# Optimization experiments

Measured on AMD Instinct MI355X. Metric: run time of the kernel, lower is better.

Reference implementation:

```python
import jax, jax.numpy as jnp
import numpy as np

Q = 127.0
EPS = 1e-8

def act_quant_per_token(x):
    # per-token absmax scale over last dim
    s = jnp.max(jnp.abs(x), axis=-1, keepdims=True) / Q
    s = jnp.maximum(s, EPS)
    xq = jnp.clip(jnp.round(x / s), -Q, Q)
    return xq * s

def ternary_quant(w):
    gamma = jnp.maximum(jnp.mean(jnp.abs(w)), 1e-6)
    wq = jnp.round(jnp.clip(w / gamma, -1.0, 1.0))
    return wq * gamma

def setup_inputs() -> dict:
    key = jax.random.key(0)
    k1, k2 = jax.random.split(key)
    x = jax.random.normal(k1, (4, 2048, 4096), dtype=jnp.float32)
    weight = jax.random.normal(k2, (16384, 4096), dtype=jnp.float32) * 0.02
    return {"x": x, "weight": weight}

def reference(x, weight):
    xq = act_quant_per_token(x)            # [B, S, D]
    wq = ternary_quant(weight)             # [O, D]
    return jnp.einsum('bsd,od->bso', xq, wq)  # [B, S, O]
```

## Files before the change

### kernel.cpp

```cpp
#include <hip/hip_runtime.h>
#include <stdint.h>


#define M_DIM 8192
#define N_DIM 16384
#define K_DIM 4096
#define W_ELEMS (N_DIM * K_DIM)
#define X_ELEMS (M_DIM * K_DIM)

typedef int v4i __attribute__((ext_vector_type(4)));

#define WS_GSUM   0u
#define WS_SCALES 256u
#define WS_XQ     65536u
#define WS_WQ     33685504u

__global__ __launch_bounds__(256) void k_gamma(const float4* __restrict__ w,
                                               double* __restrict__ gsum) {
    int tid = blockIdx.x * 256 + threadIdx.x;
    int stride = gridDim.x * 256;
    float s = 0.f;
    for (int i = tid; i < W_ELEMS / 4; i += stride) {
        float4 v = w[i];
        s += fabsf(v.x) + fabsf(v.y) + fabsf(v.z) + fabsf(v.w);
    }
    #pragma unroll
    for (int off = 32; off; off >>= 1) s += __shfl_down(s, off, 64);
    __shared__ float wsum[4];
    int lane = threadIdx.x & 63, wv = threadIdx.x >> 6;
    if (lane == 0) wsum[wv] = s;
    __syncthreads();
    if (threadIdx.x == 0) {
        double t = (double)wsum[0] + (double)wsum[1] + (double)wsum[2] + (double)wsum[3];
        atomicAdd(gsum, t);
    }
}

__device__ __forceinline__ int pack4i8(float a, float b, float c, float d) {
    int ia = (int)a & 0xFF, ib = (int)b & 0xFF, ic = (int)c & 0xFF, id = (int)d & 0xFF;
    return ia | (ib << 8) | (ic << 16) | (id << 24);
}

__global__ __launch_bounds__(256) void k_wq(const float4* __restrict__ w,
                                            const double* __restrict__ gsum,
                                            int* __restrict__ wq4) {
    float g = fmaxf((float)(*gsum * (1.0 / 67108864.0)), 1e-6f);
    int tid = blockIdx.x * 256 + threadIdx.x;
    int stride = gridDim.x * 256;
    for (int i = tid; i < W_ELEMS / 4; i += stride) {
        float4 v = w[i];
        float qa = rintf(fminf(fmaxf(v.x / g, -1.f), 1.f));
        float qb = rintf(fminf(fmaxf(v.y / g, -1.f), 1.f));
        float qc = rintf(fminf(fmaxf(v.z / g, -1.f), 1.f));
        float qd = rintf(fminf(fmaxf(v.w / g, -1.f), 1.f));
        wq4[i] = pack4i8(qa, qb, qc, qd);
    }
}

__global__ __launch_bounds__(256) void k_xq(const float4* __restrict__ x,
                                            int* __restrict__ xq4,
                                            float* __restrict__ scales) {
    int token = blockIdx.x;
    int t = threadIdx.x;
    const float4* xrow = x + (size_t)token * (K_DIM / 4);
    float4 v[4];
    float m = 0.f;
    #pragma unroll
    for (int i = 0; i < 4; i++) {
        v[i] = xrow[i * 256 + t];
        m = fmaxf(m, fmaxf(fmaxf(fabsf(v[i].x), fabsf(v[i].y)),
                           fmaxf(fabsf(v[i].z), fabsf(v[i].w))));
    }
    #pragma unroll
    for (int off = 32; off; off >>= 1) m = fmaxf(m, __shfl_xor(m, off, 64));
    __shared__ float wm[4];
    int lane = t & 63, wv = t >> 6;
    if (lane == 0) wm[wv] = m;
    __syncthreads();
    m = fmaxf(fmaxf(wm[0], wm[1]), fmaxf(wm[2], wm[3]));
    float s = fmaxf(m / 127.0f, 1e-8f);
    int* orow = xq4 + (size_t)token * (K_DIM / 4);
    #pragma unroll
    for (int i = 0; i < 4; i++) {
        float qa = fminf(fmaxf(rintf(v[i].x / s), -127.f), 127.f);
        float qb = fminf(fmaxf(rintf(v[i].y / s), -127.f), 127.f);
        float qc = fminf(fmaxf(rintf(v[i].z / s), -127.f), 127.f);
        float qd = fminf(fmaxf(rintf(v[i].w / s), -127.f), 127.f);
        orow[i * 256 + t] = pack4i8(qa, qb, qc, qd);
    }
    if (t == 0) scales[token] = s;
}

#define ASYNC_CP16(g, l)                                                              \
    __builtin_amdgcn_global_load_lds((const __attribute__((address_space(1))) void*)(g), \
                                     (__attribute__((address_space(3))) void*)(l), 16, 0, 0)

__global__ __launch_bounds__(256) void k_gemm(const char* __restrict__ A,
                                              const char* __restrict__ B,
                                              const float* __restrict__ scales,
                                              const double* __restrict__ gsum,
                                              float* __restrict__ C) {
    __shared__ char As[128 * 64];
    __shared__ char Bs[128 * 64];
    const int t = threadIdx.x;
    const int m0 = blockIdx.y * 128;
    const int n0 = blockIdx.x * 128;

    const char* aA0 = A + (size_t)(m0 + (t >> 2)) * K_DIM + (t & 3) * 16;
    const char* aA1 = A + (size_t)(m0 + 64 + (t >> 2)) * K_DIM + (t & 3) * 16;
    const char* aB0 = B + (size_t)(n0 + (t >> 2)) * K_DIM + (t & 3) * 16;
    const char* aB1 = B + (size_t)(n0 + 64 + (t >> 2)) * K_DIM + (t & 3) * 16;
    char* lA0 = &As[t * 16];
    char* lA1 = &As[4096 + t * 16];
    char* lB0 = &Bs[t * 16];
    char* lB1 = &Bs[4096 + t * 16];

    v4i acc[4][4];
    #pragma unroll
    for (int i = 0; i < 4; i++)
        #pragma unroll
        for (int j = 0; j < 4; j++) {
            v4i z = {0, 0, 0, 0};
            acc[i][j] = z;
        }

    const int lane = t & 63;
    const int wv = t >> 6;
    const int qm = (wv >> 1) * 64;
    const int qn = (wv & 1) * 64;
    const int r16 = lane & 15;
    const int kq = lane >> 4;

    for (int kk = 0; kk < K_DIM; kk += 64) {
        ASYNC_CP16(aA0 + kk, lA0);
        ASYNC_CP16(aA1 + kk, lA1);
        ASYNC_CP16(aB0 + kk, lB0);
        ASYNC_CP16(aB1 + kk, lB1);
        __syncthreads();
        v4i af[4], bf[4];
        #pragma unroll
        for (int i = 0; i < 4; i++)
            af[i] = *(const v4i*)&As[(qm + i * 16 + r16) * 64 + kq * 16];
        #pragma unroll
        for (int j = 0; j < 4; j++)
            bf[j] = *(const v4i*)&Bs[(qn + j * 16 + r16) * 64 + kq * 16];
        #pragma unroll
        for (int i = 0; i < 4; i++)
            #pragma unroll
            for (int j = 0; j < 4; j++)
                acc[i][j] = __builtin_amdgcn_mfma_i32_16x16x64_i8(af[i], bf[j], acc[i][j], 0, 0, 0);
        __syncthreads();
    }

    float gamma = fmaxf((float)(*gsum * (1.0 / 67108864.0)), 1e-6f);
    #pragma unroll
    for (int i = 0; i < 4; i++) {
        #pragma unroll
        for (int r = 0; r < 4; r++) {
            int grow = m0 + qm + i * 16 + kq * 4 + r;
            float sv = scales[grow] * gamma;
            #pragma unroll
            for (int j = 0; j < 4; j++) {
                int gcol = n0 + qn + j * 16 + r16;
                C[(size_t)grow * N_DIM + gcol] = sv * (float)acc[i][j][r];
            }
        }
    }
}

extern "C" void kernel_launch(void* const* d_in, const int* in_sizes, int n_in,
                              void* d_out, int out_size, void* d_ws, size_t ws_size,
                              hipStream_t stream) {
    const float* x = (const float*)d_in[0];
    const float* w = (const float*)d_in[1];
    float* out = (float*)d_out;
    char* ws = (char*)d_ws;

    double* gsum = (double*)(ws + WS_GSUM);
    float* scales = (float*)(ws + WS_SCALES);
    char* xq = ws + WS_XQ;
    char* wq = ws + WS_WQ;

    hipMemsetAsync(gsum, 0, sizeof(double), stream);
    k_gamma<<<2048, 256, 0, stream>>>((const float4*)w, gsum);
    k_wq<<<4096, 256, 0, stream>>>((const float4*)w, gsum, (int*)wq);
    k_xq<<<M_DIM, 256, 0, stream>>>((const float4*)x, (int*)xq, scales);
    k_gemm<<<dim3(N_DIM / 128, M_DIM / 128), 256, 0, stream>>>(xq, wq, scales, gsum, out);
}
```

Measured before the change: 1.393 ms.

## Rewrite int8 GEMM with 256x256 tiles and 4-stage async LDS pipeline

Replaces the single-buffered 128x128 int8 MFMA GEMM with a 256x256 tile computed by 8 waves, each covering 128x64. Global-to-LDS async copies are issued three k-steps ahead into a 4-deep ring buffer, with explicit vmcnt waits and raw barriers. An XOR swizzle on the LDS layout avoids bank conflicts, and MFMA phases run at raised wave priority. This aims to hide memory latency and increase operand reuse, at the cost of 128 KB of LDS per block, which limits occupancy to one block per CU.

Measured after the change: 1.279 ms. -8.2%, faster.

```diff
diff --git a/kernel.cpp b/kernel.cpp
--- a/kernel.cpp
+++ b/kernel.cpp
@@ -91,81 +91,128 @@
     if (t == 0) scales[token] = s;
 }
 
+
+#define BK 64
+#define NT (K_DIM / BK)
+
 #define ASYNC_CP16(g, l)                                                              \
     __builtin_amdgcn_global_load_lds((const __attribute__((address_space(1))) void*)(g), \
                                      (__attribute__((address_space(3))) void*)(l), 16, 0, 0)
-
-__global__ __launch_bounds__(256) void k_gemm(const char* __restrict__ A,
-                                              const char* __restrict__ B,
-                                              const float* __restrict__ scales,
-                                              const double* __restrict__ gsum,
-                                              float* __restrict__ C) {
-    __shared__ char As[128 * 64];
-    __shared__ char Bs[128 * 64];
+#define WAITV(n) asm volatile("s_waitcnt vmcnt(" #n ")" ::: "memory")
+#define BARRIER() do { asm volatile("" ::: "memory");       \
+                       __builtin_amdgcn_s_barrier();        \
+                       asm volatile("" ::: "memory"); } while (0)
+
+__global__ __launch_bounds__(512, 2) void k_gemm(const char* __restrict__ A,
+                                                 const char* __restrict__ B,
+                                                 const float* __restrict__ scales,
+                                                 const double* __restrict__ gsum,
+                                                 float* __restrict__ C) {
+    __shared__ __align__(16) char As[4][256 * BK];
+    __shared__ __align__(16) char Bs[4][256 * BK];
+
     const int t = threadIdx.x;
-    const int m0 = blockIdx.y * 128;
-    const int n0 = blockIdx.x * 128;
-
-    const char* aA0 = A + (size_t)(m0 + (t >> 2)) * K_DIM + (t & 3) * 16;
-    const char* aA1 = A + (size_t)(m0 + 64 + (t >> 2)) * K_DIM + (t & 3) * 16;
-    const char* aB0 = B + (size_t)(n0 + (t >> 2)) * K_DIM + (t & 3) * 16;
-    const char* aB1 = B + (size_t)(n0 + 64 + (t >> 2)) * K_DIM + (t & 3) * 16;
-    char* lA0 = &As[t * 16];
-    char* lA1 = &As[4096 + t * 16];
-    char* lB0 = &Bs[t * 16];
-    char* lB1 = &Bs[4096 + t * 16];
-
-    v4i acc[4][4];
-    #pragma unroll
-    for (int i = 0; i < 4; i++)
+    const int w = t >> 6;
+    const int l = t & 63;
+    const int m0 = blockIdx.y * 256;
+    const int n0 = blockIdx.x * 256;
+
+    const int srow = l >> 2;
+    const int sslot = (l & 3) ^ ((l >> 3) & 3);
+    const char* gA0 = A + (size_t)(m0 + w * 16 + srow) * K_DIM + sslot * 16;
+    const char* gA1 = gA0 + (size_t)128 * K_DIM;
+    const char* gB0 = B + (size_t)(n0 + w * 16 + srow) * K_DIM + sslot * 16;
+    const char* gB1 = gB0 + (size_t)128 * K_DIM;
+    const int ldsOff = w * 1024 + l * 16;
+
+#define STAGE_A(kt, buf) do {                              \
+        ASYNC_CP16(gA0 + (size_t)(kt) * BK, &As[buf][ldsOff]);        \
+        ASYNC_CP16(gA1 + (size_t)(kt) * BK, &As[buf][8192 + ldsOff]); } while (0)
+#define STAGE_B(kt, buf) do {                              \
+        ASYNC_CP16(gB0 + (size_t)(kt) * BK, &Bs[buf][ldsOff]);        \
+        ASYNC_CP16(gB1 + (size_t)(kt) * BK, &Bs[buf][8192 + ldsOff]); } while (0)
+
+    const int wm = w >> 2;
+    const int wn = w & 3;
+    const int r16 = l & 15;
+    const int kq = l >> 4;
+    const int swz = ((kq ^ ((r16 >> 1) & 3)) << 4);
+    const int aoff = (wm * 128 + r16) * BK + swz;
+    const int boff = (wn * 64 + r16) * BK + swz;
+
+    v4i acc[8][4];
+    #pragma unroll
+    for (int i = 0; i < 8; i++)
         #pragma unroll
         for (int j = 0; j < 4; j++) {
             v4i z = {0, 0, 0, 0};
             acc[i][j] = z;
         }
 
-    const int lane = t & 63;
-    const int wv = t >> 6;
-    const int qm = (wv >> 1) * 64;
-    const int qn = (wv & 1) * 64;
-    const int r16 = lane & 15;
-    const int kq = lane >> 4;
-
-    for (int kk = 0; kk < K_DIM; kk += 64) {
-        ASYNC_CP16(aA0 + kk, lA0);
-        ASYNC_CP16(aA1 + kk, lA1);
-        ASYNC_CP16(aB0 + kk, lB0);
-        ASYNC_CP16(aB1 + kk, lB1);
-        __syncthreads();
-        v4i af[4], bf[4];
-        #pragma unroll
-        for (int i = 0; i < 4; i++)
-            af[i] = *(const v4i*)&As[(qm + i * 16 + r16) * 64 + kq * 16];
-        #pragma unroll
-        for (int j = 0; j < 4; j++)
-            bf[j] = *(const v4i*)&Bs[(qn + j * 16 + r16) * 64 + kq * 16];
-        #pragma unroll
-        for (int i = 0; i < 4; i++)
+    STAGE_A(0, 0); STAGE_B(0, 0);
+    STAGE_A(1, 1); STAGE_B(1, 1);
+    STAGE_A(2, 2); STAGE_B(2, 2);
+    WAITV(8);
+    BARRIER();
+
+    #pragma unroll 4
+    for (int kt = 0; kt < NT; ++kt) {
+        const int buf = kt & 3;
+        const int pbuf = (kt + 3) & 3;
+        const char* as = As[buf];
+        const char* bs = Bs[buf];
+        v4i af[4], bf[4], ag[4];
+
+        if (kt < NT - 3) STAGE_A(kt + 3, pbuf);
+        #pragma unroll
+        for (int i = 0; i < 4; ++i) af[i] = *(const v4i*)&as[aoff + i * 1024];
+        #pragma unroll
+        for (int j = 0; j < 4; ++j) bf[j] = *(const v4i*)&bs[boff + j * 1024];
+        BARRIER();
+        __builtin_amdgcn_s_setprio(1);
+        #pragma unroll
+        for (int i = 0; i < 4; ++i)
             #pragma unroll
-            for (int j = 0; j < 4; j++)
+            for (int j = 0; j < 4; ++j)
                 acc[i][j] = __builtin_amdgcn_mfma_i32_16x16x64_i8(af[i], bf[j], acc[i][j], 0, 0, 0);
-        __syncthreads();
-    }
-
-    float gamma = fmaxf((float)(*gsum * (1.0 / 67108864.0)), 1e-6f);
-    #pragma unroll
-    for (int i = 0; i < 4; i++) {
-        #pragma unroll
-        for (int r = 0; r < 4; r++) {
-            int grow = m0 + qm + i * 16 + kq * 4 + r;
-            float sv = scales[grow] * gamma;
+        __builtin_amdgcn_s_setprio(0);
+        BARRIER();
+
+        if (kt < NT - 3) STAGE_B(kt + 3, pbuf);
+        #pragma unroll
+        for (int i = 0; i < 4; ++i) ag[i] = *(const v4i*)&as[aoff + 4096 + i * 1024];
+        BARRIER();
+        __builtin_amdgcn_s_setprio(1);
+        #pragma unroll
+        for (int i = 0; i < 4; ++i)
             #pragma unroll
-            for (int j = 0; j < 4; j++) {
-                int gcol = n0 + qn + j * 16 + r16;
+            for (int j = 0; j < 4; ++j)
+                acc[4 + i][j] = __builtin_amdgcn_mfma_i32_16x16x64_i8(ag[i], bf[j], acc[4 + i][j], 0, 0, 0);
+        __builtin_amdgcn_s_setprio(0);
+
+        if (kt < NT - 3)       { WAITV(8); }
+        else if (kt == NT - 3) { WAITV(4); }
+        else if (kt == NT - 2) { WAITV(0); }
+        if (kt < NT - 1) BARRIER();
+    }
+
+    const float gamma = fmaxf((float)(*gsum * (1.0 / 67108864.0)), 1e-6f);
+    #pragma unroll
+    for (int i = 0; i < 8; ++i) {
+        const int brow = m0 + wm * 128 + i * 16 + kq * 4;
+        #pragma unroll
+        for (int r = 0; r < 4; ++r) {
+            const int grow = brow + r;
+            const float sv = scales[grow] * gamma;
+            #pragma unroll
+            for (int j = 0; j < 4; ++j) {
+                const int gcol = n0 + wn * 64 + j * 16 + r16;
                 C[(size_t)grow * N_DIM + gcol] = sv * (float)acc[i][j][r];
             }
         }
     }
+#undef STAGE_A
+#undef STAGE_B
 }
 
 extern "C" void kernel_launch(void* const* d_in, const int* in_sizes, int n_in,
@@ -185,5 +232,5 @@
     k_gamma<<<2048, 256, 0, stream>>>((const float4*)w, gsum);
     k_wq<<<4096, 256, 0, stream>>>((const float4*)w, gsum, (int*)wq);
     k_xq<<<M_DIM, 256, 0, stream>>>((const float4*)x, (int*)xq, scales);
-    k_gemm<<<dim3(N_DIM / 128, M_DIM / 128), 256, 0, stream>>>(xq, wq, scales, gsum, out);
-}
+    k_gemm<<<dim3(N_DIM / 256, M_DIM / 256), 512, 0, stream>>>(xq, wq, scales, gsum, out);
+}
```
